# Optimization experiments

Hardware: AMD Instinct MI355X
Metric: run time of the kernel (lower is better)

## Reference

```python
import jax, jax.numpy as jnp
import numpy as np

B, S, D = 2, 2048, 1024
QH, KVH, DH = 16, 4, 64
TOP_K = 128
ROPE_BASE = 10000.0


def _rope(x):
    # x: [B, H, S, DH]; standard LLaMA-style rotate-half RoPE, no freq scaling
    half = DH // 2
    inv_freq = 1.0 / (ROPE_BASE ** (jnp.arange(half, dtype=jnp.float32) / half))
    ang = jnp.arange(S, dtype=jnp.float32)[:, None] * inv_freq[None, :]  # [S, half]
    cos, sin = jnp.cos(ang), jnp.sin(ang)
    x1, x2 = x[..., :half], x[..., half:]
    return jnp.concatenate([x1 * cos - x2 * sin, x2 * cos + x1 * sin], axis=-1)


def setup_inputs() -> dict:
    key = jax.random.key(0)
    ks = jax.random.split(key, 5)
    return {
        "x": jax.random.normal(ks[0], (B, S, D), dtype=jnp.float32),
        "Wq": jax.random.normal(ks[1], (QH * DH, D), dtype=jnp.float32) * 0.02,
        "Wk": jax.random.normal(ks[2], (KVH * DH, D), dtype=jnp.float32) * 0.02,
        "Wv": jax.random.normal(ks[3], (KVH * DH, D), dtype=jnp.float32) * 0.02,
        "Wo": jax.random.normal(ks[4], (D, QH * DH), dtype=jnp.float32) * 0.02,
    }


def reference(x, Wq, Wk, Wv, Wo):
    # projections (Linear, no bias): y = x @ W.T
    q = (x @ Wq.T).reshape(B, S, QH, DH).transpose(0, 2, 1, 3)   # [B,QH,S,DH]
    k = (x @ Wk.T).reshape(B, S, KVH, DH).transpose(0, 2, 1, 3)  # [B,KVH,S,DH]
    v = (x @ Wv.T).reshape(B, S, KVH, DH).transpose(0, 2, 1, 3)
    q = _rope(q)
    k = _rope(k)
    # repeat_kv: GQA expand kv heads to q heads
    rep = QH // KVH
    k = jnp.repeat(k, rep, axis=1)
    v = jnp.repeat(v, rep, axis=1)
    scores = jnp.einsum("bhqd,bhkd->bhqk", q, k) / np.sqrt(DH)  # [B,QH,S,S]
    causal = jnp.triu(jnp.ones((S, S), dtype=bool), k=1)
    scores = jnp.where(causal, -jnp.inf, scores)
    # top-k masking before softmax: keep entries >= per-row k-th largest score
    top_vals = jax.lax.top_k(scores, TOP_K)[0]        # [B,QH,S,TOP_K]
    thr = top_vals[..., -1:]
    scores = jnp.where(scores < thr, -jnp.inf, scores)
    w = jax.nn.softmax(scores, axis=-1)
    out = jnp.einsum("bhqk,bhkd->bhqd", w, v)         # [B,QH,S,DH]
    out = out.transpose(0, 2, 1, 3).reshape(B, S, QH * DH)
    return out @ Wo.T
```

## Files before the change

### kernel.cpp

```cpp
#include <hip/hip_runtime.h>
#include <hip/hip_bf16.h>
#include <hip/hip_fp16.h>
#include <math.h>

constexpr int cB   = 2;
constexpr int cS   = 2048;
constexpr int cD   = 1024;
constexpr int cQH  = 16;
constexpr int cKVH = 4;
constexpr int cDH  = 64;
constexpr int cTOPK = 128;
constexpr int cM   = cB * cS;
constexpr int cNB  = cS / 64;
constexpr int cLSZ = 384;

constexpr int cTI  = 16;
constexpr int cSTR = 258;

constexpr int cNQ  = cQH * cDH;
constexpr int cNK  = cKVH * cDH;
constexpr int cNQKV = cNQ + 2 * cNK;
constexpr int cVC0 = cNQ + cNK;

typedef __attribute__((ext_vector_type(8))) short short8;
typedef __attribute__((ext_vector_type(4))) float floatx4;
typedef _Float16 half8 __attribute__((ext_vector_type(8)));

__device__ inline ushort f2bf(float f) {
    unsigned u = __float_as_uint(f);
    return (ushort)((u + 0x7FFFu + ((u >> 16) & 1u)) >> 16);
}

__device__ __forceinline__ void glds16(const ushort* g, ushort* l) {
    __builtin_amdgcn_global_load_lds(
        (const __attribute__((address_space(1))) unsigned int*)g,
        (__attribute__((address_space(3))) unsigned int*)l, 16, 0, 0);
}

constexpr int cE0 = cM * cD;
constexpr int cE1 = cE0 + cNQ * cD;
constexpr int cE2 = cE1 + cNK * cD;
constexpr int cE3 = cE2 + cNK * cD;
constexpr int cE4 = cE3 + cD * cQH * cDH;

__global__ void cast_all_bf16(const float* __restrict__ x,
                              const float* __restrict__ wq,
                              const float* __restrict__ wk,
                              const float* __restrict__ wv,
                              const float* __restrict__ wo,
                              ushort* __restrict__ dst) {
    const int i4 = (blockIdx.x * blockDim.x + threadIdx.x) * 4;
    if (i4 >= cE4) return;
    const float* s;
    int off;
    if (i4 < cE0)      { s = x;  off = i4; }
    else if (i4 < cE1) { s = wq; off = i4 - cE0; }
    else if (i4 < cE2) { s = wk; off = i4 - cE1; }
    else if (i4 < cE3) { s = wv; off = i4 - cE2; }
    else               { s = wo; off = i4 - cE3; }
    const float4 v = *(const float4*)(s + off);
    ushort4 r;
    r.x = f2bf(v.x); r.y = f2bf(v.y); r.z = f2bf(v.z); r.w = f2bf(v.w);
    *(ushort4*)(dst + i4) = r;
}

__global__ void build_trig(float* __restrict__ ct, float* __restrict__ st) {
    const int idx = blockIdx.x * blockDim.x + threadIdx.x;
    if (idx >= cS * 32) return;
    const int d = idx & 31;
    const int s = idx >> 5;
    const float inv_freq = powf(10000.0f, -(float)d / 32.0f);
    const float ang = (float)s * inv_freq;
    ct[idx] = cosf(ang);
    st[idx] = sinf(ang);
}

__global__ __launch_bounds__(256) void gemm_bf16_bt(
        const ushort* __restrict__ A, const ushort* __restrict__ W,
        float* __restrict__ C, int M, int N, int K) {
    __shared__ ushort AsL[128 * 32];
    __shared__ ushort BsL[128 * 32];

    const int tid  = threadIdx.x;
    const int lane = tid & 63;
    const int w    = tid >> 6;
    const int wm   = (w & 1) * 64;
    const int wn   = (w >> 1) * 64;
    const int m0   = blockIdx.y * 128;
    const int n0   = blockIdx.x * 128;
    const int quad = lane >> 4;
    const int l16  = lane & 15;

    int r0, q0, r1, q1;
    {
        const int g5 = (w * 128 + lane) & 31;
        const int b4 = (g5 >> 4) & 1, b3 = (g5 >> 3) & 1, b2 = (g5 >> 2) & 1;
        const int b1 = (g5 >> 1) & 1, b0 = g5 & 1;
        r0 = ((w * 128 + lane) >> 5) * 8 + ((b4 << 2) | (b3 << 1) | (b2 ^ b4));
        q0 = ((b1 ^ b3) << 1) | (b0 ^ b2 ^ b4);
    }
    {
        const int gI = w * 128 + 64 + lane;
        const int g5 = gI & 31;
        const int b4 = (g5 >> 4) & 1, b3 = (g5 >> 3) & 1, b2 = (g5 >> 2) & 1;
        const int b1 = (g5 >> 1) & 1, b0 = g5 & 1;
        r1 = (gI >> 5) * 8 + ((b4 << 2) | (b3 << 1) | (b2 ^ b4));
        q1 = ((b1 ^ b3) << 1) | (b0 ^ b2 ^ b4);
    }
    const size_t aOff0 = (size_t)(m0 + r0) * K + q0 * 8;
    const size_t aOff1 = (size_t)(m0 + r1) * K + q1 * 8;
    const size_t bOff0 = (size_t)(n0 + r0) * K + q0 * 8;
    const size_t bOff1 = (size_t)(n0 + r1) * K + q1 * 8;
    ushort* ldsA0 = AsL + w * 1024;
    ushort* ldsA1 = AsL + w * 1024 + 512;
    ushort* ldsB0 = BsL + w * 1024;
    ushort* ldsB1 = BsL + w * 1024 + 512;

    int eA[4], eB[4];
    #pragma unroll
    for (int mi = 0; mi < 4; ++mi) {
        const int rr = wm + mi * 16 + l16;
        eA[mi] = (((rr >> 3) * 32) + ((4 * (rr & 7) + quad) ^ (rr & 7))) * 8;
    }
    #pragma unroll
    for (int ni = 0; ni < 4; ++ni) {
        const int rn = wn + ni * 16 + l16;
        eB[ni] = (((rn >> 3) * 32) + ((4 * (rn & 7) + quad) ^ (rn & 7))) * 8;
    }

    floatx4 acc[4][4];
    #pragma unroll
    for (int mi = 0; mi < 4; ++mi)
        #pragma unroll
        for (int ni = 0; ni < 4; ++ni)
            acc[mi][ni] = (floatx4){0.f, 0.f, 0.f, 0.f};

    for (int k0 = 0; k0 < K; k0 += 32) {
        glds16(A + aOff0 + k0, ldsA0);
        glds16(A + aOff1 + k0, ldsA1);
        glds16(W + bOff0 + k0, ldsB0);
        glds16(W + bOff1 + k0, ldsB1);
        __syncthreads();

        short8 af[4], bf[4];
        #pragma unroll
        for (int mi = 0; mi < 4; ++mi)
            af[mi] = *(const short8*)(AsL + eA[mi]);
        #pragma unroll
        for (int ni = 0; ni < 4; ++ni)
            bf[ni] = *(const short8*)(BsL + eB[ni]);
        #pragma unroll
        for (int mi = 0; mi < 4; ++mi)
            #pragma unroll
            for (int ni = 0; ni < 4; ++ni)
                acc[mi][ni] = __builtin_amdgcn_mfma_f32_16x16x32_bf16(
                    af[mi], bf[ni], acc[mi][ni], 0, 0, 0);
        __syncthreads();
    }

    #pragma unroll
    for (int mi = 0; mi < 4; ++mi)
        #pragma unroll
        for (int ni = 0; ni < 4; ++ni)
            #pragma unroll
            for (int r = 0; r < 4; ++r) {
                const int row = m0 + wm + mi * 16 + quad * 4 + r;
                const int col = n0 + wn + ni * 16 + l16;
                C[(size_t)row * N + col] = acc[mi][ni][r];
            }
}

__global__ __launch_bounds__(256) void gemm_qkv_rope(
        const ushort* __restrict__ A, const ushort* __restrict__ W,
        ushort* __restrict__ qff, ushort* __restrict__ kff,
        ushort* __restrict__ vff,
        const float* __restrict__ ct, const float* __restrict__ st) {
    __shared__ ushort AsL[128 * 32];
    __shared__ ushort BsL[128 * 32];

    constexpr int K = cD;
    const int tid  = threadIdx.x;
    const int lane = tid & 63;
    const int w    = tid >> 6;
    const int wm   = (w & 1) * 64;
    const int wn   = (w >> 1) * 64;
    const int m0   = blockIdx.y * 128;
    const int n0   = blockIdx.x * 128;
    const int quad = lane >> 4;
    const int l16  = lane & 15;

    int r0, q0, r1, q1;
    {
        const int g5 = (w * 128 + lane) & 31;
        const int b4 = (g5 >> 4) & 1, b3 = (g5 >> 3) & 1, b2 = (g5 >> 2) & 1;
        const int b1 = (g5 >> 1) & 1, b0 = g5 & 1;
        r0 = ((w * 128 + lane) >> 5) * 8 + ((b4 << 2) | (b3 << 1) | (b2 ^ b4));
        q0 = ((b1 ^ b3) << 1) | (b0 ^ b2 ^ b4);
    }
    {
        const int gI = w * 128 + 64 + lane;
        const int g5 = gI & 31;
        const int b4 = (g5 >> 4) & 1, b3 = (g5 >> 3) & 1, b2 = (g5 >> 2) & 1;
        const int b1 = (g5 >> 1) & 1, b0 = g5 & 1;
        r1 = (gI >> 5) * 8 + ((b4 << 2) | (b3 << 1) | (b2 ^ b4));
        q1 = ((b1 ^ b3) << 1) | (b0 ^ b2 ^ b4);
    }
    const size_t aOff0 = (size_t)(m0 + r0) * K + q0 * 8;
    const size_t aOff1 = (size_t)(m0 + r1) * K + q1 * 8;
    const size_t bOff0 = (size_t)(n0 + r0) * K + q0 * 8;
    const size_t bOff1 = (size_t)(n0 + r1) * K + q1 * 8;
    ushort* ldsA0 = AsL + w * 1024;
    ushort* ldsA1 = AsL + w * 1024 + 512;
    ushort* ldsB0 = BsL + w * 1024;
    ushort* ldsB1 = BsL + w * 1024 + 512;

    int eA[4], eB[4];
    #pragma unroll
    for (int mi = 0; mi < 4; ++mi) {
        const int rr = wm + mi * 16 + l16;
        eA[mi] = (((rr >> 3) * 32) + ((4 * (rr & 7) + quad) ^ (rr & 7))) * 8;
    }
    #pragma unroll
    for (int ni = 0; ni < 4; ++ni) {
        const int rn = wn + ni * 16 + l16;
        eB[ni] = (((rn >> 3) * 32) + ((4 * (rn & 7) + quad) ^ (rn & 7))) * 8;
    }

    floatx4 acc[4][4];
    #pragma unroll
    for (int mi = 0; mi < 4; ++mi)
        #pragma unroll
        for (int ni = 0; ni < 4; ++ni)
            acc[mi][ni] = (floatx4){0.f, 0.f, 0.f, 0.f};

    for (int k0 = 0; k0 < K; k0 += 32) {
        glds16(A + aOff0 + k0, ldsA0);
        glds16(A + aOff1 + k0, ldsA1);
        glds16(W + bOff0 + k0, ldsB0);
        glds16(W + bOff1 + k0, ldsB1);
        __syncthreads();

        short8 af[4], bf[4];
        #pragma unroll
        for (int mi = 0; mi < 4; ++mi)
            af[mi] = *(const short8*)(AsL + eA[mi]);
        #pragma unroll
        for (int ni = 0; ni < 4; ++ni)
            bf[ni] = *(const short8*)(BsL + eB[ni]);
        #pragma unroll
        for (int mi = 0; mi < 4; ++mi)
            #pragma unroll
            for (int ni = 0; ni < 4; ++ni)
                acc[mi][ni] = __builtin_amdgcn_mfma_f32_16x16x32_bf16(
                    af[mi], bf[ni], acc[mi][ni], 0, 0, 0);
        __syncthreads();
    }

    const int colBase = n0 + wn;
    if (colBase < cNQ) {
        const int h = colBase >> 6;
        #pragma unroll
        for (int ni = 0; ni < 2; ++ni) {
            const int d = ni * 16 + l16;
            #pragma unroll
            for (int mi = 0; mi < 4; ++mi)
                #pragma unroll
                for (int r = 0; r < 4; ++r) {
                    const int row = m0 + wm + mi * 16 + quad * 4 + r;
                    const int s   = row & (cS - 1);
                    const float c  = ct[(s << 5) + d];
                    const float si = st[(s << 5) + d];
                    const float x1 = acc[mi][ni][r];
                    const float x2 = acc[mi][ni + 2][r];
                    const float o1 = (x1 * c - x2 * si) * 0.125f;
                    const float o2 = (x2 * c + x1 * si) * 0.125f;
                    ushort* o = qff + ((size_t)row * cQH + h) * cDH + d;
                    o[0]  = __builtin_bit_cast(ushort, (_Float16)o1);
                    o[32] = __builtin_bit_cast(ushort, (_Float16)o2);
                }
        }
    } else if (colBase < cVC0) {
        const int h = (colBase - cNQ) >> 6;
        #pragma unroll
        for (int ni = 0; ni < 2; ++ni) {
            const int d = ni * 16 + l16;
            #pragma unroll
            for (int mi = 0; mi < 4; ++mi)
                #pragma unroll
                for (int r = 0; r < 4; ++r) {
                    const int row = m0 + wm + mi * 16 + quad * 4 + r;
                    const int s   = row & (cS - 1);
                    const float c  = ct[(s << 5) + d];
                    const float si = st[(s << 5) + d];
                    const float x1 = acc[mi][ni][r];
                    const float x2 = acc[mi][ni + 2][r];
                    const float o1 = (x1 * c - x2 * si) * 1.0f;
                    const float o2 = (x2 * c + x1 * si) * 1.0f;
                    ushort* o = kff + ((size_t)row * cKVH + h) * cDH + d;
                    o[0]  = __builtin_bit_cast(ushort, (_Float16)o1);
                    o[32] = __builtin_bit_cast(ushort, (_Float16)o2);
                }
        }
    } else {
        const int h = (colBase - cVC0) >> 6;
        #pragma unroll
        for (int ni = 0; ni < 4; ++ni) {
            const int d = ni * 16 + l16;
            #pragma unroll
            for (int mi = 0; mi < 4; ++mi)
                #pragma unroll
                for (int r = 0; r < 4; ++r) {
                    const int row = m0 + wm + mi * 16 + quad * 4 + r;
                    vff[((size_t)row * cKVH + h) * cDH + d] =
                        __builtin_bit_cast(ushort, (_Float16)acc[mi][ni][r]);
                }
        }
    }
}

__device__ inline unsigned fmap(float f) {
    unsigned u = __float_as_uint(f);
    return (u & 0x80000000u) ? ~u : (u | 0x80000000u);
}
__device__ inline float funmap(unsigned u) {
    unsigned v = (u & 0x80000000u) ? (u & 0x7FFFFFFFu) : ~u;
    return __uint_as_float(v);
}

__global__ __launch_bounds__(1024) void attn_tile_kernel(
        const ushort* __restrict__ qf, const ushort* __restrict__ kf,
        const ushort* __restrict__ vf, ushort* __restrict__ out) {
    extern __shared__ char smem[];
    unsigned* stg = (unsigned*)smem;
    unsigned* klA = (unsigned*)smem;
    int*      jlA = (int*)(klA + cTI * cLSZ);

    const int lane = threadIdx.x & 63;
    const int wv   = __builtin_amdgcn_readfirstlane(threadIdx.x >> 6);

    const int x  = blockIdx.x;
    const int it = (cS / cTI - 1) - (x >> 5);
    const int bh = x & 31;
    const int h  = bh & 15;
    const int b  = bh >> 4;
    const int kvh = h >> 2;
    const int i0  = it * cTI;

    const size_t bS = (size_t)b * cS;
    const int l16   = lane & 15;
    const int quad  = lane >> 4;
    const int jperm = ((lane & 3) << 4) + (lane >> 2);
    const int i     = i0 + wv;

    const ushort* qp = qf + ((bS + i0 + l16) * cQH + h) * cDH + quad * 8;
    const half8 a0h = __builtin_bit_cast(half8, *(const uint4*)qp);
    const half8 a1h = __builtin_bit_cast(half8, *(const uint4*)(qp + 32));

    unsigned key[cNB];
    #pragma unroll
    for (int jb = 0; jb < cNB; ++jb) key[jb] = 0u;

    const int nk16   = it + 1;
    const int nchunk = (nk16 + 15) >> 4;

    #pragma unroll
    for (int c = 0; c < 8; ++c) {
        if (c >= nchunk) break;
        const int kb16 = (c << 4) + wv;
        if (kb16 < nk16) {
            const ushort* kp = kf + ((bS + (kb16 << 4) + l16) * cKVH + kvh) * cDH + quad * 8;
            const uint4 b0 = *(const uint4*)kp;
            const uint4 b1 = *(const uint4*)(kp + 32);
            floatx4 acc = (floatx4){0.f, 0.f, 0.f, 0.f};
            acc = __builtin_amdgcn_mfma_f32_16x16x32_f16(
                a0h, __builtin_bit_cast(half8, b0), acc, 0, 0, 0);
            acc = __builtin_amdgcn_mfma_f32_16x16x32_f16(
                a1h, __builtin_bit_cast(half8, b1), acc, 0, 0, 0);
            const int jg = (kb16 << 4) + l16;
            unsigned* sp = stg + (c & 1) * (cTI * cSTR) + (wv << 4) + l16;
            #pragma unroll
            for (int r2 = 0; r2 < 4; ++r2) {
                const int qrow = quad * 4 + r2;
                sp[qrow * cSTR] = (jg <= i0 + qrow) ? fmap(acc[r2]) : 0u;
            }
        }
        __syncthreads();
        {
            const unsigned* rp = stg + (c & 1) * (cTI * cSTR) + wv * cSTR;
            #pragma unroll
            for (int jj = 0; jj < 4; ++jj) {
                const int j = (c << 8) + (jj << 6) + jperm;
                const unsigned kr = rp[(jj << 6) + jperm];
                key[(c << 2) + jj] = (j <= i) ? kr : 0u;
            }
        }
    }
    __syncthreads();

    const int nb = (i >> 6) + 1;
    unsigned* kl = klA + wv * cLSZ;
    int*      jl = jlA + wv * cLSZ;
    const int vbase0 = (int)(((unsigned)bS * cKVH + kvh) * cDH);

    unsigned um = 0u, un = 0xFFFFFFFFu;
    #pragma unroll
    for (int jb = 0; jb < cNB; ++jb) {
        if (jb >= nb) break;
        const unsigned kk = key[jb];
        um = max(um, kk);
        un = min(un, kk ? kk : 0xFFFFFFFFu);
    }
    #pragma unroll
    for (int off = 32; off >= 1; off >>= 1) {
        um = max(um, (unsigned)__shfl_xor((int)um, off));
        un = min(un, (unsigned)__shfl_xor((int)un, off));
    }
    const float mrow = funmap(um);

    unsigned ustar;
    if (i < cTOPK) {
        ustar = un;
    } else {
        unsigned lo = un, hi = um;
        while (lo < hi) {
            const unsigned d   = hi - lo;
            const unsigned mid = lo + (d >> 1) + (d & 1u);
            int cnt2 = 0;
            #pragma unroll
            for (int jb = 0; jb < cNB; ++jb) {
                if (jb >= nb) break;
                cnt2 += __popcll(__ballot(key[jb] >= mid));
            }
            if (cnt2 == cTOPK) {
                unsigned mn = 0xFFFFFFFFu;
                #pragma unroll
                for (int jb = 0; jb < cNB; ++jb) {
                    if (jb >= nb) break;
                    const unsigned kk = key[jb];
                    mn = min(mn, (kk >= mid) ? kk : 0xFFFFFFFFu);
                }
                #pragma unroll
                for (int off = 32; off >= 1; off >>= 1)
                    mn = min(mn, (unsigned)__shfl_xor((int)mn, off));
                lo = mn;
                break;
            }
            if (cnt2 > cTOPK) lo = mid; else hi = mid - 1u;
        }
        ustar = lo;
    }

    const unsigned long long mlt = (1ull << lane) - 1ull;
    int base = 0;
    #pragma unroll
    for (int jb = 0; jb < cNB; ++jb) {
        if (jb >= nb) break;
        const int j = (jb << 6) + jperm;
        const bool keep = (j <= i) && (key[jb] >= ustar);
        const unsigned long long mk = __ballot(keep);
        const int pos = base + __popcll(mk & mlt);
        if (keep && pos < cLSZ) {
            kl[pos] = key[jb];
            jl[pos] = vbase0 + j * (cKVH * cDH);
        }
        base += __popcll(mk);
    }
    const int cnt = min(base, cLSZ);

    float zp = 0.f;
    for (int t = lane; t < cnt; t += 64) {
        const float s  = funmap(kl[t]);
        const float wt = __expf(s - mrow);
        ((float*)kl)[t] = wt;
        zp += wt;
    }
    #pragma unroll
    for (int off = 32; off >= 1; off >>= 1) zp += __shfl_xor(zp, off);
    const float invZ = 1.0f / zp;

    float ac0 = 0.f, ac1 = 0.f, ac2 = 0.f, ac3 = 0.f;
    float ac4 = 0.f, ac5 = 0.f, ac6 = 0.f, ac7 = 0.f;
    int t = 0;
    #pragma unroll 2
    for (; t + 7 < cnt; t += 8) {
        const float wt0 = ((float*)kl)[t];
        const float wt1 = ((float*)kl)[t + 1];
        const float wt2 = ((float*)kl)[t + 2];
        const float wt3 = ((float*)kl)[t + 3];
        const float wt4 = ((float*)kl)[t + 4];
        const float wt5 = ((float*)kl)[t + 5];
        const float wt6 = ((float*)kl)[t + 6];
        const float wt7 = ((float*)kl)[t + 7];
        const int vo0 = jl[t];
        const int vo1 = jl[t + 1];
        const int vo2 = jl[t + 2];
        const int vo3 = jl[t + 3];
        const int vo4 = jl[t + 4];
        const int vo5 = jl[t + 5];
        const int vo6 = jl[t + 6];
        const int vo7 = jl[t + 7];
        ac0 += wt0 * (float)__builtin_bit_cast(_Float16, vf[vo0 + lane]);
        ac1 += wt1 * (float)__builtin_bit_cast(_Float16, vf[vo1 + lane]);
        ac2 += wt2 * (float)__builtin_bit_cast(_Float16, vf[vo2 + lane]);
        ac3 += wt3 * (float)__builtin_bit_cast(_Float16, vf[vo3 + lane]);
        ac4 += wt4 * (float)__builtin_bit_cast(_Float16, vf[vo4 + lane]);
        ac5 += wt5 * (float)__builtin_bit_cast(_Float16, vf[vo5 + lane]);
        ac6 += wt6 * (float)__builtin_bit_cast(_Float16, vf[vo6 + lane]);
        ac7 += wt7 * (float)__builtin_bit_cast(_Float16, vf[vo7 + lane]);
    }
    for (; t < cnt; ++t) {
        const float wt = ((float*)kl)[t];
        const int   vo = jl[t];
        ac0 += wt * (float)__builtin_bit_cast(_Float16, vf[vo + lane]);
    }
    const float acc = ((ac0 + ac1) + (ac2 + ac3)) + ((ac4 + ac5) + (ac6 + ac7));
    out[((bS + i) * cQH + h) * cDH + lane] = f2bf(acc * invZ);
}

extern "C" void kernel_launch(void* const* d_in, const int* in_sizes, int n_in,
                              void* d_out, int out_size, void* d_ws, size_t ws_size,
                              hipStream_t stream) {
    const float* x  = (const float*)d_in[0];
    const float* Wq = (const float*)d_in[1];
    const float* Wk = (const float*)d_in[2];
    const float* Wv = (const float*)d_in[3];
    const float* Wo = (const float*)d_in[4];
    float* out = (float*)d_out;

    ushort* xh   = (ushort*)d_ws;
    ushort* Wqh  = xh  + (size_t)cM * cD;
    ushort* Wkh  = Wqh + (size_t)cNQ * cD;
    ushort* Wvh  = Wkh + (size_t)cNK * cD;
    ushort* Woh  = Wvh + (size_t)cNK * cD;
    ushort* abh  = Woh + (size_t)cD * cQH * cDH;
    ushort* qff  = abh + (size_t)cM * cQH * cDH;
    ushort* kff  = qff + (size_t)cM * cQH * cDH;
    ushort* vff  = kff + (size_t)cM * cKVH * cDH;
    float*  ct   = (float*)(vff + (size_t)cM * cKVH * cDH);
    float*  st   = ct + (size_t)cS * 32;

    dim3 blk(256);

    cast_all_bf16<<<(cE4 / 4 + 255) / 256, blk, 0, stream>>>(
        x, Wq, Wk, Wv, Wo, xh);

    build_trig<<<(cS * 32 + 255) / 256, blk, 0, stream>>>(ct, st);

    gemm_qkv_rope<<<dim3(cNQKV / 128, cM / 128), blk, 0, stream>>>(
        xh, Wqh, qff, kff, vff, ct, st);

    constexpr size_t aSMEM = (size_t)cTI * cLSZ * 8;
    static_assert(2 * cTI * cSTR * 4 <= (int)aSMEM, "staging must fit");
    attn_tile_kernel<<<dim3(32 * (cS / cTI)), dim3(1024), aSMEM, stream>>>(
        qff, kff, vff, abh);

    gemm_bf16_bt<<<dim3(cD / 128, cM / 128), blk, 0, stream>>>(abh, Woh, out, cM, cD, cD);
}
```

Baseline: 502.0 us.

## Pair long and short causal query tiles per attention block; fuse cast and trig kernels

Each attention block now processes two 16-row query tiles, tile 127-p and tile p, so every block does about the same causal work. The grid shrinks from 4096 to 2048 blocks and a barrier separates the two tiles, which share LDS. Separately, the bf16 cast and RoPE trig table kernels are merged into one launch to save a kernel launch. The gain depends on whether load balancing beats the loss of parallelism and the serialized second pass.

```diff
diff --git a/kernel.cpp b/kernel.cpp
--- a/kernel.cpp
+++ b/kernel.cpp
@@ -42,37 +42,41 @@
 constexpr int cE2 = cE1 + cNK * cD;
 constexpr int cE3 = cE2 + cNK * cD;
 constexpr int cE4 = cE3 + cD * cQH * cDH;
-
-__global__ void cast_all_bf16(const float* __restrict__ x,
-                              const float* __restrict__ wq,
-                              const float* __restrict__ wk,
-                              const float* __restrict__ wv,
-                              const float* __restrict__ wo,
-                              ushort* __restrict__ dst) {
-    const int i4 = (blockIdx.x * blockDim.x + threadIdx.x) * 4;
-    if (i4 >= cE4) return;
-    const float* s;
-    int off;
-    if (i4 < cE0)      { s = x;  off = i4; }
-    else if (i4 < cE1) { s = wq; off = i4 - cE0; }
-    else if (i4 < cE2) { s = wk; off = i4 - cE1; }
-    else if (i4 < cE3) { s = wv; off = i4 - cE2; }
-    else               { s = wo; off = i4 - cE3; }
-    const float4 v = *(const float4*)(s + off);
-    ushort4 r;
-    r.x = f2bf(v.x); r.y = f2bf(v.y); r.z = f2bf(v.z); r.w = f2bf(v.w);
-    *(ushort4*)(dst + i4) = r;
-}
-
-__global__ void build_trig(float* __restrict__ ct, float* __restrict__ st) {
+constexpr int cCAST4 = cE4 / 4;
+constexpr int cTRIG  = cS * 32;
+
+__global__ void cast_all_bf16_trig(const float* __restrict__ x,
+                                   const float* __restrict__ wq,
+                                   const float* __restrict__ wk,
+                                   const float* __restrict__ wv,
+                                   const float* __restrict__ wo,
+                                   ushort* __restrict__ dst,
+                                   float* __restrict__ ct,
+                                   float* __restrict__ st) {
     const int idx = blockIdx.x * blockDim.x + threadIdx.x;
-    if (idx >= cS * 32) return;
-    const int d = idx & 31;
-    const int s = idx >> 5;
+    if (idx < cCAST4) {
+        const int i4 = idx * 4;
+        const float* s;
+        int off;
+        if (i4 < cE0)      { s = x;  off = i4; }
+        else if (i4 < cE1) { s = wq; off = i4 - cE0; }
+        else if (i4 < cE2) { s = wk; off = i4 - cE1; }
+        else if (i4 < cE3) { s = wv; off = i4 - cE2; }
+        else               { s = wo; off = i4 - cE3; }
+        const float4 v = *(const float4*)(s + off);
+        ushort4 r;
+        r.x = f2bf(v.x); r.y = f2bf(v.y); r.z = f2bf(v.z); r.w = f2bf(v.w);
+        *(ushort4*)(dst + i4) = r;
+        return;
+    }
+    const int t = idx - cCAST4;
+    if (t >= cTRIG) return;
+    const int d = t & 31;
+    const int s = t >> 5;
     const float inv_freq = powf(10000.0f, -(float)d / 32.0f);
     const float ang = (float)s * inv_freq;
-    ct[idx] = cosf(ang);
-    st[idx] = sinf(ang);
+    ct[t] = cosf(ang);
+    st[t] = sinf(ang);
 }
 
 __global__ __launch_bounds__(256) void gemm_bf16_bt(
@@ -339,182 +343,188 @@
     const int wv   = __builtin_amdgcn_readfirstlane(threadIdx.x >> 6);
 
     const int x  = blockIdx.x;
-    const int it = (cS / cTI - 1) - (x >> 5);
+    const int p  = x >> 5;
     const int bh = x & 31;
     const int h  = bh & 15;
     const int b  = bh >> 4;
     const int kvh = h >> 2;
-    const int i0  = it * cTI;
 
     const size_t bS = (size_t)b * cS;
     const int l16   = lane & 15;
     const int quad  = lane >> 4;
     const int jperm = ((lane & 3) << 4) + (lane >> 2);
-    const int i     = i0 + wv;
-
-    const ushort* qp = qf + ((bS + i0 + l16) * cQH + h) * cDH + quad * 8;
-    const half8 a0h = __builtin_bit_cast(half8, *(const uint4*)qp);
-    const half8 a1h = __builtin_bit_cast(half8, *(const uint4*)(qp + 32));
-
-    unsigned key[cNB];
-    #pragma unroll
-    for (int jb = 0; jb < cNB; ++jb) key[jb] = 0u;
-
-    const int nk16   = it + 1;
-    const int nchunk = (nk16 + 15) >> 4;
-
-    #pragma unroll
-    for (int c = 0; c < 8; ++c) {
-        if (c >= nchunk) break;
-        const int kb16 = (c << 4) + wv;
-        if (kb16 < nk16) {
-            const ushort* kp = kf + ((bS + (kb16 << 4) + l16) * cKVH + kvh) * cDH + quad * 8;
-            const uint4 b0 = *(const uint4*)kp;
-            const uint4 b1 = *(const uint4*)(kp + 32);
-            floatx4 acc = (floatx4){0.f, 0.f, 0.f, 0.f};
-            acc = __builtin_amdgcn_mfma_f32_16x16x32_f16(
-                a0h, __builtin_bit_cast(half8, b0), acc, 0, 0, 0);
-            acc = __builtin_amdgcn_mfma_f32_16x16x32_f16(
-                a1h, __builtin_bit_cast(half8, b1), acc, 0, 0, 0);
-            const int jg = (kb16 << 4) + l16;
-            unsigned* sp = stg + (c & 1) * (cTI * cSTR) + (wv << 4) + l16;
-            #pragma unroll
-            for (int r2 = 0; r2 < 4; ++r2) {
-                const int qrow = quad * 4 + r2;
-                sp[qrow * cSTR] = (jg <= i0 + qrow) ? fmap(acc[r2]) : 0u;
-            }
-        }
-        __syncthreads();
-        {
-            const unsigned* rp = stg + (c & 1) * (cTI * cSTR) + wv * cSTR;
-            #pragma unroll
-            for (int jj = 0; jj < 4; ++jj) {
-                const int j = (c << 8) + (jj << 6) + jperm;
-                const unsigned kr = rp[(jj << 6) + jperm];
-                key[(c << 2) + jj] = (j <= i) ? kr : 0u;
-            }
-        }
-    }
-    __syncthreads();
-
-    const int nb = (i >> 6) + 1;
+    const int vbase0 = (int)(((unsigned)bS * cKVH + kvh) * cDH);
     unsigned* kl = klA + wv * cLSZ;
     int*      jl = jlA + wv * cLSZ;
-    const int vbase0 = (int)(((unsigned)bS * cKVH + kvh) * cDH);
-
-    unsigned um = 0u, un = 0xFFFFFFFFu;
-    #pragma unroll
-    for (int jb = 0; jb < cNB; ++jb) {
-        if (jb >= nb) break;
-        const unsigned kk = key[jb];
-        um = max(um, kk);
-        un = min(un, kk ? kk : 0xFFFFFFFFu);
-    }
-    #pragma unroll
-    for (int off = 32; off >= 1; off >>= 1) {
-        um = max(um, (unsigned)__shfl_xor((int)um, off));
-        un = min(un, (unsigned)__shfl_xor((int)un, off));
-    }
-    const float mrow = funmap(um);
-
-    unsigned ustar;
-    if (i < cTOPK) {
-        ustar = un;
-    } else {
-        unsigned lo = un, hi = um;
-        while (lo < hi) {
-            const unsigned d   = hi - lo;
-            const unsigned mid = lo + (d >> 1) + (d & 1u);
-            int cnt2 = 0;
-            #pragma unroll
-            for (int jb = 0; jb < cNB; ++jb) {
-                if (jb >= nb) break;
-                cnt2 += __popcll(__ballot(key[jb] >= mid));
+
+    for (int tsel = 0; tsel < 2; ++tsel) {
+        if (tsel == 1) __syncthreads();
+
+        const int it = tsel ? p : (127 - p);
+        const int i0 = it * cTI;
+        const int i  = i0 + wv;
+
+        const ushort* qp = qf + ((bS + i0 + l16) * cQH + h) * cDH + quad * 8;
+        const half8 a0h = __builtin_bit_cast(half8, *(const uint4*)qp);
+        const half8 a1h = __builtin_bit_cast(half8, *(const uint4*)(qp + 32));
+
+        unsigned key[cNB];
+        #pragma unroll
+        for (int jb = 0; jb < cNB; ++jb) key[jb] = 0u;
+
+        const int nk16   = it + 1;
+        const int nchunk = (nk16 + 15) >> 4;
+
+        #pragma unroll
+        for (int c = 0; c < 8; ++c) {
+            if (c >= nchunk) break;
+            const int kb16 = (c << 4) + wv;
+            if (kb16 < nk16) {
+                const ushort* kp = kf + ((bS + (kb16 << 4) + l16) * cKVH + kvh) * cDH + quad * 8;
+                const uint4 b0 = *(const uint4*)kp;
+                const uint4 b1 = *(const uint4*)(kp + 32);
+                floatx4 acc = (floatx4){0.f, 0.f, 0.f, 0.f};
+                acc = __builtin_amdgcn_mfma_f32_16x16x32_f16(
+                    a0h, __builtin_bit_cast(half8, b0), acc, 0, 0, 0);
+                acc = __builtin_amdgcn_mfma_f32_16x16x32_f16(
+                    a1h, __builtin_bit_cast(half8, b1), acc, 0, 0, 0);
+                const int jg = (kb16 << 4) + l16;
+                unsigned* sp = stg + (c & 1) * (cTI * cSTR) + (wv << 4) + l16;
+                #pragma unroll
+                for (int r2 = 0; r2 < 4; ++r2) {
+                    const int qrow = quad * 4 + r2;
+                    sp[qrow * cSTR] = (jg <= i0 + qrow) ? fmap(acc[r2]) : 0u;
+                }
             }
-            if (cnt2 == cTOPK) {
-                unsigned mn = 0xFFFFFFFFu;
+            __syncthreads();
+            {
+                const unsigned* rp = stg + (c & 1) * (cTI * cSTR) + wv * cSTR;
+                #pragma unroll
+                for (int jj = 0; jj < 4; ++jj) {
+                    const int j = (c << 8) + (jj << 6) + jperm;
+                    const unsigned kr = rp[(jj << 6) + jperm];
+                    key[(c << 2) + jj] = (j <= i) ? kr : 0u;
+                }
+            }
+        }
+        __syncthreads();
+
+        const int nb = (i >> 6) + 1;
+
+        unsigned um = 0u, un = 0xFFFFFFFFu;
+        #pragma unroll
+        for (int jb = 0; jb < cNB; ++jb) {
+            if (jb >= nb) break;
+            const unsigned kk = key[jb];
+            um = max(um, kk);
+            un = min(un, kk ? kk : 0xFFFFFFFFu);
+        }
+        #pragma unroll
+        for (int off = 32; off >= 1; off >>= 1) {
+            um = max(um, (unsigned)__shfl_xor((int)um, off));
+            un = min(un, (unsigned)__shfl_xor((int)un, off));
+        }
+        const float mrow = funmap(um);
+
+        unsigned ustar;
+        if (i < cTOPK) {
+            ustar = un;
+        } else {
+            unsigned lo = un, hi = um;
+            while (lo < hi) {
+                const unsigned d   = hi - lo;
+                const unsigned mid = lo + (d >> 1) + (d & 1u);
+                int cnt2 = 0;
                 #pragma unroll
                 for (int jb = 0; jb < cNB; ++jb) {
                     if (jb >= nb) break;
-                    const unsigned kk = key[jb];
-                    mn = min(mn, (kk >= mid) ? kk : 0xFFFFFFFFu);
-                }
-                #pragma unroll
-                for (int off = 32; off >= 1; off >>= 1)
-                    mn = min(mn, (unsigned)__shfl_xor((int)mn, off));
-                lo = mn;
-                break;
+                    cnt2 += __popcll(__ballot(key[jb] >= mid));
+                }
+                if (cnt2 == cTOPK) {
+                    unsigned mn = 0xFFFFFFFFu;
+                    #pragma unroll
+                    for (int jb = 0; jb < cNB; ++jb) {
+                        if (jb >= nb) break;
+                        const unsigned kk = key[jb];
+                        mn = min(mn, (kk >= mid) ? kk : 0xFFFFFFFFu);
+                    }
+                    #pragma unroll
+                    for (int off = 32; off >= 1; off >>= 1)
+                        mn = min(mn, (unsigned)__shfl_xor((int)mn, off));
+                    lo = mn;
+                    break;
+                }
+                if (cnt2 > cTOPK) lo = mid; else hi = mid - 1u;
             }
-            if (cnt2 > cTOPK) lo = mid; else hi = mid - 1u;
-        }
-        ustar = lo;
-    }
-
-    const unsigned long long mlt = (1ull << lane) - 1ull;
-    int base = 0;
-    #pragma unroll
-    for (int jb = 0; jb < cNB; ++jb) {
-        if (jb >= nb) break;
-        const int j = (jb << 6) + jperm;
-        const bool keep = (j <= i) && (key[jb] >= ustar);
-        const unsigned long long mk = __ballot(keep);
-        const int pos = base + __popcll(mk & mlt);
-        if (keep && pos < cLSZ) {
-            kl[pos] = key[jb];
-            jl[pos] = vbase0 + j * (cKVH * cDH);
-        }
-        base += __popcll(mk);
-    }
-    const int cnt = min(base, cLSZ);
-
-    float zp = 0.f;
-    for (int t = lane; t < cnt; t += 64) {
-        const float s  = funmap(kl[t]);
-        const float wt = __expf(s - mrow);
-        ((float*)kl)[t] = wt;
-        zp += wt;
-    }
-    #pragma unroll
-    for (int off = 32; off >= 1; off >>= 1) zp += __shfl_xor(zp, off);
-    const float invZ = 1.0f / zp;
-
-    float ac0 = 0.f, ac1 = 0.f, ac2 = 0.f, ac3 = 0.f;
-    float ac4 = 0.f, ac5 = 0.f, ac6 = 0.f, ac7 = 0.f;
-    int t = 0;
-    #pragma unroll 2
-    for (; t + 7 < cnt; t += 8) {
-        const float wt0 = ((float*)kl)[t];
-        const float wt1 = ((float*)kl)[t + 1];
-        const float wt2 = ((float*)kl)[t + 2];
-        const float wt3 = ((float*)kl)[t + 3];
-        const float wt4 = ((float*)kl)[t + 4];
-        const float wt5 = ((float*)kl)[t + 5];
-        const float wt6 = ((float*)kl)[t + 6];
-        const float wt7 = ((float*)kl)[t + 7];
-        const int vo0 = jl[t];
-        const int vo1 = jl[t + 1];
-        const int vo2 = jl[t + 2];
-        const int vo3 = jl[t + 3];
-        const int vo4 = jl[t + 4];
-        const int vo5 = jl[t + 5];
-        const int vo6 = jl[t + 6];
-        const int vo7 = jl[t + 7];
-        ac0 += wt0 * (float)__builtin_bit_cast(_Float16, vf[vo0 + lane]);
-        ac1 += wt1 * (float)__builtin_bit_cast(_Float16, vf[vo1 + lane]);
-        ac2 += wt2 * (float)__builtin_bit_cast(_Float16, vf[vo2 + lane]);
-        ac3 += wt3 * (float)__builtin_bit_cast(_Float16, vf[vo3 + lane]);
-        ac4 += wt4 * (float)__builtin_bit_cast(_Float16, vf[vo4 + lane]);
-        ac5 += wt5 * (float)__builtin_bit_cast(_Float16, vf[vo5 + lane]);
-        ac6 += wt6 * (float)__builtin_bit_cast(_Float16, vf[vo6 + lane]);
-        ac7 += wt7 * (float)__builtin_bit_cast(_Float16, vf[vo7 + lane]);
-    }
-    for (; t < cnt; ++t) {
-        const float wt = ((float*)kl)[t];
-        const int   vo = jl[t];
-        ac0 += wt * (float)__builtin_bit_cast(_Float16, vf[vo + lane]);
-    }
-    const float acc = ((ac0 + ac1) + (ac2 + ac3)) + ((ac4 + ac5) + (ac6 + ac7));
-    out[((bS + i) * cQH + h) * cDH + lane] = f2bf(acc * invZ);
+            ustar = lo;
+        }
+
+        const unsigned long long mlt = (1ull << lane) - 1ull;
+        int base = 0;
+        #pragma unroll
+        for (int jb = 0; jb < cNB; ++jb) {
+            if (jb >= nb) break;
+            const int j = (jb << 6) + jperm;
+            const bool keep = (j <= i) && (key[jb] >= ustar);
+            const unsigned long long mk = __ballot(keep);
+            const int pos = base + __popcll(mk & mlt);
+            if (keep && pos < cLSZ) {
+                kl[pos] = key[jb];
+                jl[pos] = vbase0 + j * (cKVH * cDH);
+            }
+            base += __popcll(mk);
+        }
+        const int cnt = min(base, cLSZ);
+
+        float zp = 0.f;
+        for (int t = lane; t < cnt; t += 64) {
+            const float s  = funmap(kl[t]);
+            const float wt = __expf(s - mrow);
+            ((float*)kl)[t] = wt;
+            zp += wt;
+        }
+        #pragma unroll
+        for (int off = 32; off >= 1; off >>= 1) zp += __shfl_xor(zp, off);
+        const float invZ = 1.0f / zp;
+
+        float ac0 = 0.f, ac1 = 0.f, ac2 = 0.f, ac3 = 0.f;
+        float ac4 = 0.f, ac5 = 0.f, ac6 = 0.f, ac7 = 0.f;
+        int t = 0;
+        #pragma unroll 2
+        for (; t + 7 < cnt; t += 8) {
+            const float wt0 = ((float*)kl)[t];
+            const float wt1 = ((float*)kl)[t + 1];
+            const float wt2 = ((float*)kl)[t + 2];
+            const float wt3 = ((float*)kl)[t + 3];
+            const float wt4 = ((float*)kl)[t + 4];
+            const float wt5 = ((float*)kl)[t + 5];
+            const float wt6 = ((float*)kl)[t + 6];
+            const float wt7 = ((float*)kl)[t + 7];
+            const int vo0 = jl[t];
+            const int vo1 = jl[t + 1];
+            const int vo2 = jl[t + 2];
+            const int vo3 = jl[t + 3];
+            const int vo4 = jl[t + 4];
+            const int vo5 = jl[t + 5];
+            const int vo6 = jl[t + 6];
+            const int vo7 = jl[t + 7];
+            ac0 += wt0 * (float)__builtin_bit_cast(_Float16, vf[vo0 + lane]);
+            ac1 += wt1 * (float)__builtin_bit_cast(_Float16, vf[vo1 + lane]);
+            ac2 += wt2 * (float)__builtin_bit_cast(_Float16, vf[vo2 + lane]);
+            ac3 += wt3 * (float)__builtin_bit_cast(_Float16, vf[vo3 + lane]);
+            ac4 += wt4 * (float)__builtin_bit_cast(_Float16, vf[vo4 + lane]);
+            ac5 += wt5 * (float)__builtin_bit_cast(_Float16, vf[vo5 + lane]);
+            ac6 += wt6 * (float)__builtin_bit_cast(_Float16, vf[vo6 + lane]);
+            ac7 += wt7 * (float)__builtin_bit_cast(_Float16, vf[vo7 + lane]);
+        }
+        for (; t < cnt; ++t) {
+            const float wt = ((float*)kl)[t];
+            const int   vo = jl[t];
+            ac0 += wt * (float)__builtin_bit_cast(_Float16, vf[vo + lane]);
+        }
+        const float acc = ((ac0 + ac1) + (ac2 + ac3)) + ((ac4 + ac5) + (ac6 + ac7));
+        out[((bS + i) * cQH + h) * cDH + lane] = f2bf(acc * invZ);
+    }
 }
 
 extern "C" void kernel_launch(void* const* d_in, const int* in_sizes, int n_in,
@@ -541,17 +551,15 @@
 
     dim3 blk(256);
 
-    cast_all_bf16<<<(cE4 / 4 + 255) / 256, blk, 0, stream>>>(
-        x, Wq, Wk, Wv, Wo, xh);
-
-    build_trig<<<(cS * 32 + 255) / 256, blk, 0, stream>>>(ct, st);
+    cast_all_bf16_trig<<<(cCAST4 + cTRIG + 255) / 256, blk, 0, stream>>>(
+        x, Wq, Wk, Wv, Wo, xh, ct, st);
 
     gemm_qkv_rope<<<dim3(cNQKV / 128, cM / 128), blk, 0, stream>>>(
         xh, Wqh, qff, kff, vff, ct, st);
 
     constexpr size_t aSMEM = (size_t)cTI * cLSZ * 8;
     static_assert(2 * cTI * cSTR * 4 <= (int)aSMEM, "staging must fit");
-    attn_tile_kernel<<<dim3(32 * (cS / cTI)), dim3(1024), aSMEM, stream>>>(
+    attn_tile_kernel<<<dim3(32 * 64), dim3(1024), aSMEM, stream>>>(
         qff, kff, vff, abh);
 
     gemm_bf16_bt<<<dim3(cD / 128, cM / 128), blk, 0, stream>>>(abh, Woh, out, cM, cD, cD);
```

New measurement: 715.1 us. 42.5% more time.
